# Performance work log

Measured on AMD Instinct MI355X. Metric: run time of the kernel, lower is better.

The kernel has to match this reference:

```python
import jax, jax.numpy as jnp
import numpy as np
from jax import lax


def setup_inputs() -> dict:
    key = jax.random.key(0)
    x = jax.random.normal(key, (8, 128, 256, 256), dtype=jnp.float32)
    return {"x": x}


def reference(x) -> jnp.ndarray:
    # Vertical line (corner-style) pool: running maximum along the vertical
    # (H) axis, scanning from bottom to top, i.e. out[..., i, :] = max_{j>=i} x[..., j, :].
    # Implemented as an associative scan with max, reversed along axis=2 (H of NCHW).
    return lax.associative_scan(jnp.maximum, x, axis=2, reverse=True)
```

## Files before the change

### kernel.cpp

```cpp
#include <hip/hip_runtime.h>
#include <hip/hip_bf16.h>
#include <math.h>


#define H 256
#define W 256

__global__ __launch_bounds__(256) void VerticalLinePool_kernel(
    const float* __restrict__ x, float* __restrict__ out) {
    const int w = threadIdx.x;
    const size_t base = (size_t)blockIdx.x * (H * W) + w;
    const float* __restrict__ xp = x + base;
    float* __restrict__ op = out + base;

    float acc = -INFINITY;
#pragma unroll 8
    for (int h = H - 1; h >= 0; --h) {
        float v = xp[(size_t)h * W];
        acc = fmaxf(acc, v);
        op[(size_t)h * W] = acc;
    }
}

extern "C" void kernel_launch(void* const* d_in, const int* in_sizes, int n_in,
                              void* d_out, int out_size, void* d_ws, size_t ws_size,
                              hipStream_t stream) {
    const float* x = (const float*)d_in[0];
    float* out = (float*)d_out;
    const int slabs = in_sizes[0] / (H * W);
    VerticalLinePool_kernel<<<slabs, 256, 0, stream>>>(x, out);
}
```

Baseline: 435.5 us.

## Split vertical scan into four row chunks combined via shared-memory carries

Each block now covers a 64-column strip of a slab, and each of its four waves handles a 64-row chunk. Every wave computes a local suffix max held in registers, chunk totals are exchanged through shared memory, and the outputs are fixed up with the max of the later chunks. The point is to break the serial 256-step dependent chain and to put many independent loads in flight per thread, using 4x more blocks. Loads and stores are also nontemporal. The cost is 64 registers per thread for the buffered chunk, a block barrier, and 256-byte row segments per wave instead of 1 KB rows.

```diff
diff --git a/kernel.cpp b/kernel.cpp
--- a/kernel.cpp
+++ b/kernel.cpp
@@ -5,20 +5,45 @@
 
 #define H 256
 #define W 256
+#define CH 64
+
+typedef float f32;
 
 __global__ __launch_bounds__(256) void VerticalLinePool_kernel(
     const float* __restrict__ x, float* __restrict__ out) {
-    const int w = threadIdx.x;
-    const size_t base = (size_t)blockIdx.x * (H * W) + w;
-    const float* __restrict__ xp = x + base;
-    float* __restrict__ op = out + base;
+    const int tid = threadIdx.x;
+    const int c  = tid >> 6;
+    const int wl = tid & 63;
+    const int q    = blockIdx.x & 3;
+    const int slab = blockIdx.x >> 2;
 
-    float acc = -INFINITY;
-#pragma unroll 8
-    for (int h = H - 1; h >= 0; --h) {
-        float v = xp[(size_t)h * W];
-        acc = fmaxf(acc, v);
-        op[(size_t)h * W] = acc;
+    const size_t col = (size_t)slab * (H * W) + (size_t)q * 64 + wl;
+    const float* __restrict__ xp = x + col;
+    float* __restrict__ op = out + col;
+
+    const int h0 = c * CH;
+
+    float s[CH];
+    float run = -INFINITY;
+#pragma unroll
+    for (int i = CH - 1; i >= 0; --i) {
+        float v = __builtin_nontemporal_load(&xp[(size_t)(h0 + i) * W]);
+        run = fmaxf(run, v);
+        s[i] = run;
+    }
+
+    __shared__ float tot[4][64];
+    tot[c][wl] = run;
+    __syncthreads();
+
+    float M = -INFINITY;
+    if (c < 3) M = tot[c + 1][wl];
+    if (c < 2) M = fmaxf(M, tot[c + 2][wl]);
+    if (c < 1) M = fmaxf(M, tot[c + 3][wl]);
+
+#pragma unroll
+    for (int i = 0; i < CH; ++i) {
+        __builtin_nontemporal_store(fmaxf(s[i], M), &op[(size_t)(h0 + i) * W]);
     }
 }
 
@@ -28,5 +53,5 @@
     const float* x = (const float*)d_in[0];
     float* out = (float*)d_out;
     const int slabs = in_sizes[0] / (H * W);
-    VerticalLinePool_kernel<<<slabs, 256, 0, stream>>>(x, out);
+    VerticalLinePool_kernel<<<slabs * 4, 256, 0, stream>>>(x, out);
 }
```

Result: faster. 423.9 us (-2.7%).
